# Optimization experiments

Measured on AMD Instinct MI355X. Metric: run time of the kernel, lower is better.

## Reference

```python
import jax, jax.numpy as jnp
import numpy as np

DEGREE = 3
N_KNOTS = 5

def _bspline_basis(x, t_ext, degree):
    """Vectorized Cox-de Boor. x: (..., ), t_ext: (m,) extended knots.
    Returns (..., m-1-degree) degree-`degree` basis values."""
    xe = x[..., None]
    # order-0 indicator basis: (..., m-1)
    B = ((xe >= t_ext[:-1]) & (xe < t_ext[1:])).astype(x.dtype)
    for p in range(1, degree + 1):
        left_den = t_ext[p:-1] - t_ext[:-(p + 1)]
        right_den = t_ext[p + 1:] - t_ext[1:-p]
        left = jnp.where(left_den > 0,
                         (xe - t_ext[:-(p + 1)]) / jnp.where(left_den > 0, left_den, 1.0),
                         0.0) * B[..., :-1]
        right = jnp.where(right_den > 0,
                          (t_ext[p + 1:] - xe) / jnp.where(right_den > 0, right_den, 1.0),
                          0.0) * B[..., 1:]
        B = left + right
    return B

def setup_inputs() -> dict:
    key = jax.random.key(0)
    k1, k2, k3, k4 = jax.random.split(key, 4)
    batch, input_dim, out_dim = 16384, 4096, 64
    n_coeff = N_KNOTS - DEGREE  # 2
    return {
        "x": jax.random.normal(k1, (batch, input_dim), dtype=jnp.float32),
        "c": jax.random.normal(k2, (input_dim, out_dim, n_coeff), dtype=jnp.float32),
        "ws": jax.random.normal(k3, (input_dim, out_dim), dtype=jnp.float32),
        "wb": jax.random.normal(k4, (input_dim, out_dim), dtype=jnp.float32),
    }

def reference(x, c, ws, wb):
    t = jnp.linspace(-1.0, 1.0, N_KNOTS, dtype=x.dtype)
    t_ext = jnp.concatenate([t, t[-1:]])  # pad so basis count == n_knots - degree
    # B: (batch, input_dim, n_coeff); basis depends only on x, shared knots
    B = _bspline_basis(x, t_ext, DEGREE)
    spline = jnp.einsum('bik,ijk->bj', B, c * ws[:, :, None])
    silu_mix = jax.nn.silu(x) @ wb  # sum_i wb[i,j] * x_i*sigmoid(x_i)
    return spline + silu_mix
```

## Files before the change

kernel.cpp:

```cpp
#include <hip/hip_runtime.h>
#include <hip/hip_bf16.h>
#include <stdint.h>

#define BATCH   16384
#define IN_DIM  4096
#define OUT_DIM 64
#define MTILES  (BATCH/64)

#define KI2     32
#define NCH2    (IN_DIM/KI2)
#define SPLITK  8
#define CPB2    (NCH2/SPLITK)
#define GRAN2   (OUT_DIM*13)
#define CH2W    (GRAN2*8)

#define KI      64
#define KCH     (3*KI)
#define NCHUNK  (IN_DIM/KI)
#define FCPB    16
#define CHW     (OUT_DIM*KCH)

typedef __attribute__((ext_vector_type(8))) short   short8;
typedef __attribute__((ext_vector_type(4))) float   floatx4;
typedef __attribute__((ext_vector_type(4))) uint32_t uintx4;

static __device__ __forceinline__ unsigned short f2bf(float f) {
    union { float f; uint32_t u; } v; v.f = f;
    uint32_t r = v.u + 0x7FFFu + ((v.u >> 16) & 1u);
    return (unsigned short)(r >> 16);
}

static __device__ __forceinline__ uint32_t pk2bf(float lo, float hi) {
    union { float f; uint32_t u; } a, b;
    a.f = lo; b.f = hi;
    uint32_t ra = a.u + 0x7FFFu + ((a.u >> 16) & 1u);
    uint32_t rb = b.u + 0x7FFFu + ((b.u >> 16) & 1u);
    return (ra >> 16) | (rb & 0xFFFF0000u);
}

static __device__ __forceinline__ void kan_features(float xv, float& b0, float& b1, float& sl) {
    float ax  = fabsf(xv);
    float axc = fminf(ax, 1.0f);
    float a2  = axc*axc;
    float om  = 1.0f - axc;
    float inner = __builtin_fmaf(__builtin_fmaf(4.0f, axc, -4.0f), a2, (2.0f/3.0f));
    float outer = (om*om) * (om * (4.0f/3.0f));
    b0 = (axc < 0.5f) ? inner : outer;
    float xc  = fminf(fmaxf(xv, -0.5f), 1.0f);
    float c3  = (xc < 0.0f) ? (4.0f/3.0f) : (-14.0f/3.0f);
    float mid = __builtin_fmaf(__builtin_fmaf(__builtin_fmaf(c3, xc, 2.0f), xc, 1.0f), xc, (1.0f/6.0f));
    float hi  = __builtin_fmaf(__builtin_fmaf(__builtin_fmaf(22.0f, xc, -48.0f), xc, 30.0f), xc, -4.0f) * (1.0f/3.0f);
    b1 = (xc < 0.5f) ? mid : hi;
    float e = __expf(-xv);
    sl = xv * __builtin_amdgcn_rcpf(1.0f + e);
}

__global__ __launch_bounds__(256) void kan_prep(
        const float* __restrict__ c, const float* __restrict__ ws,
        const float* __restrict__ wb, unsigned short* __restrict__ Wt) {
    int idx = blockIdx.x * 256 + threadIdx.x;
    int row = idx >> 9;
    int i   = (idx & 511) << 3;
    int j   = row / 3;
    int t   = row - j*3;
    int ci  = i >> 5;
    int ig  = (i & 31) >> 3;
    unsigned short pk[8];
    #pragma unroll
    for (int e = 0; e < 8; e++) {
        int ii = i + e;
        float v;
        if (t < 2) v = c[(size_t)ii*(OUT_DIM*2) + j*2 + t] * ws[(size_t)ii*OUT_DIM + j];
        else       v = wb[(size_t)ii*OUT_DIM + j];
        pk[e] = f2bf(v);
    }
    uintx4 d;
    d[0] = pk[0] | ((uint32_t)pk[1] << 16);
    d[1] = pk[2] | ((uint32_t)pk[3] << 16);
    d[2] = pk[4] | ((uint32_t)pk[5] << 16);
    d[3] = pk[6] | ((uint32_t)pk[7] << 16);
    int g = j*13 + t*4 + ig;
    *(uintx4*)(Wt + (size_t)ci*CH2W + (size_t)g*8) = d;
}

__global__ __launch_bounds__(256, 6) void kan_main_pre(
    const float* __restrict__ x, const unsigned short* __restrict__ Wt,
    float* __restrict__ pbuf)
{
    __shared__ unsigned short Bs[2][CH2W];

    const int tid  = threadIdx.x;
    const int wave = tid >> 6;
    const int lane = tid & 63;
    const int m    = lane & 15;
    const int q    = lane >> 4;
    const int mt   = blockIdx.x & (MTILES - 1);
    const int kh   = blockIdx.x >> 8;
    const int row0 = mt * 64;
    const int r    = row0 + wave*16 + m;
    const float* xrow = x + (size_t)r * IN_DIM;
    const int ci0 = kh * CPB2;

    floatx4 acc[4] = {};

    floatx4 xv0 = *(const floatx4*)(xrow + ci0*KI2 + q*8);
    floatx4 xv1 = *(const floatx4*)(xrow + ci0*KI2 + q*8 + 4);

    {
        const unsigned short* gW = Wt + (size_t)ci0 * CH2W;
        #pragma unroll
        for (int p = 0; p < 3; p++) {
            int g0 = p*256 + wave*64;
            __builtin_amdgcn_global_load_lds(
                (__attribute__((address_space(1))) void*)(gW + (size_t)(g0 + lane)*8),
                (__attribute__((address_space(3))) void*)(&Bs[0][0] + (size_t)g0*8),
                16, 0, 0);
        }
        if (tid < 64)
            __builtin_amdgcn_global_load_lds(
                (__attribute__((address_space(1))) void*)(gW + (size_t)(768 + lane)*8),
                (__attribute__((address_space(3))) void*)(&Bs[0][0] + (size_t)768*8),
                16, 0, 0);
    }
    __syncthreads();

    for (int cc = 0; cc < CPB2; cc++) {
        const int buf = cc & 1;
        const int ci  = ci0 + cc;

        if (cc + 1 < CPB2) {
            const unsigned short* gW = Wt + (size_t)(ci + 1) * CH2W;
            #pragma unroll
            for (int p = 0; p < 3; p++) {
                int g0 = p*256 + wave*64;
                __builtin_amdgcn_global_load_lds(
                    (__attribute__((address_space(1))) void*)(gW + (size_t)(g0 + lane)*8),
                    (__attribute__((address_space(3))) void*)(&Bs[buf^1][0] + (size_t)g0*8),
                    16, 0, 0);
            }
            if (tid < 64)
                __builtin_amdgcn_global_load_lds(
                    (__attribute__((address_space(1))) void*)(gW + (size_t)(768 + lane)*8),
                    (__attribute__((address_space(3))) void*)(&Bs[buf^1][0] + (size_t)768*8),
                    16, 0, 0);
        }

        const int inx = (cc + 1 < CPB2) ? (ci + 1)*KI2 : ci*KI2;
        floatx4 xn0 = *(const floatx4*)(xrow + inx + q*8);
        floatx4 xn1 = *(const floatx4*)(xrow + inx + q*8 + 4);

        uintx4 afu[3];
        #pragma unroll
        for (int w = 0; w < 4; w++) {
            float v0 = (w < 2) ? xv0[w*2]     : xv1[(w-2)*2];
            float v1 = (w < 2) ? xv0[w*2 + 1] : xv1[(w-2)*2 + 1];
            float b00, b10, s0, b01, b11, s1;
            kan_features(v0, b00, b10, s0);
            kan_features(v1, b01, b11, s1);
            afu[0][w] = pk2bf(b00, b01);
            afu[1][w] = pk2bf(b10, b11);
            afu[2][w] = pk2bf(s0, s1);
        }

        #pragma unroll
        for (int t = 0; t < 3; t++) {
            #pragma unroll
            for (int n = 0; n < 4; n++) {
                const int j = n*16 + m;
                short8 bf = *(const short8*)&Bs[buf][(size_t)(j*13 + t*4 + q)*8];
                acc[n] = __builtin_amdgcn_mfma_f32_16x16x32_bf16(
                    __builtin_bit_cast(short8, afu[t]), bf, acc[n], 0, 0, 0);
            }
        }

        xv0 = xn0; xv1 = xn1;
        __syncthreads();
    }

    float* pb = pbuf + (((size_t)kh*MTILES + mt)*4)*1024;
    #pragma unroll
    for (int n = 0; n < 4; n++)
        *(floatx4*)(pb + ((size_t)n*256 + tid)*4) = acc[n];
}

__global__ __launch_bounds__(256) void kan_reduce(
    const float* __restrict__ pbuf, float* __restrict__ out)
{
    const int mt   = blockIdx.x;
    const int tid  = threadIdx.x;
    const int wave = tid >> 6;
    const int lane = tid & 63;
    const int m    = lane & 15;
    const int q    = lane >> 4;
    #pragma unroll
    for (int n = 0; n < 4; n++) {
        floatx4 s = {};
        #pragma unroll
        for (int p = 0; p < SPLITK; p++) {
            floatx4 v = *(const floatx4*)(pbuf +
                (((size_t)p*MTILES + mt)*4 + n)*1024 + (size_t)tid*4);
            s += v;
        }
        #pragma unroll
        for (int reg = 0; reg < 4; reg++) {
            int orow = mt*64 + wave*16 + q*4 + reg;
            out[(size_t)orow*OUT_DIM + n*16 + m] = s[reg];
        }
    }
}

__global__ __launch_bounds__(256, 4) void kan_main_fb(
    const float* __restrict__ x, const float* __restrict__ c,
    const float* __restrict__ ws, const float* __restrict__ wb,
    float* __restrict__ out)
{
    __shared__ unsigned short Bsf[CHW];
    const int tid  = threadIdx.x;
    const int wave = tid >> 6;
    const int lane = tid & 63;
    const int m    = lane & 15;
    const int q    = lane >> 4;
    const int mt   = blockIdx.x & (MTILES - 1);
    const int kh   = blockIdx.x >> 8;
    const int row0 = mt * 64;
    const int r    = row0 + wave*16 + m;
    const float* xrow = x + (size_t)r * IN_DIM;
    floatx4 acc[4] = {};
    for (int cc = 0; cc < FCPB; cc++) {
        const int i0 = (kh * FCPB + cc) * KI;
        floatx4 xv[4];
        xv[0] = *(const floatx4*)(xrow + i0 + q*8);
        xv[1] = *(const floatx4*)(xrow + i0 + q*8 + 4);
        xv[2] = *(const floatx4*)(xrow + i0 + 32 + q*8);
        xv[3] = *(const floatx4*)(xrow + i0 + 32 + q*8 + 4);
        uintx4 afu[6];
        #pragma unroll
        for (int g = 0; g < 2; g++) {
            #pragma unroll
            for (int w = 0; w < 4; w++) {
                float v0 = xv[g*2 + (w >> 1)][(w & 1)*2 + 0];
                float v1 = xv[g*2 + (w >> 1)][(w & 1)*2 + 1];
                float b00, b10, sl0, b01, b11, sl1;
                kan_features(v0, b00, b10, sl0);
                kan_features(v1, b01, b11, sl1);
                afu[0 + g][w] = pk2bf(b00, b01);
                afu[2 + g][w] = pk2bf(b10, b11);
                afu[4 + g][w] = pk2bf(sl0, sl1);
            }
        }
        __syncthreads();
        #pragma unroll
        for (int p = 0; p < 16; p++) {
            int idx = tid + p*256;
            int j = idx & 63, i = idx >> 6;
            int gi = i0 + i;
            const float* cp = c + ((size_t)gi*OUT_DIM + j)*2;
            float c0 = cp[0], c1 = cp[1];
            float sw = ws[(size_t)gi*OUT_DIM + j];
            float b  = wb[(size_t)gi*OUT_DIM + j];
            int jx = j & 7;
            Bsf[j*KCH + ((0*8 + (i>>3)) ^ jx)*8 + (i&7)] = f2bf(c0*sw);
            Bsf[j*KCH + ((1*8 + (i>>3)) ^ jx)*8 + (i&7)] = f2bf(c1*sw);
            Bsf[j*KCH + ((2*8 + (i>>3)) ^ jx)*8 + (i&7)] = f2bf(b);
        }
        __syncthreads();
        #pragma unroll
        for (int s = 0; s < 6; s++) {
            const int kb = (s >> 1)*8 + (s & 1)*4 + q;
            #pragma unroll
            for (int n = 0; n < 4; n++) {
                const int j = n*16 + m;
                short8 bf = *(const short8*)&Bsf[j*KCH + ((kb ^ (j & 7)) << 3)];
                acc[n] = __builtin_amdgcn_mfma_f32_16x16x32_bf16(
                    __builtin_bit_cast(short8, afu[s]), bf, acc[n], 0, 0, 0);
            }
        }
    }
    #pragma unroll
    for (int n = 0; n < 4; n++)
        #pragma unroll
        for (int reg = 0; reg < 4; reg++) {
            int orow = row0 + wave*16 + q*4 + reg;
            atomicAdd(&out[(size_t)orow*OUT_DIM + n*16 + m], acc[n][reg]);
        }
}

extern "C" void kernel_launch(void* const* d_in, const int* in_sizes, int n_in,
                              void* d_out, int out_size, void* d_ws, size_t ws_size,
                              hipStream_t stream) {
    const float* x  = (const float*)d_in[0];
    const float* c  = (const float*)d_in[1];
    const float* ws = (const float*)d_in[2];
    const float* wb = (const float*)d_in[3];
    float* out = (float*)d_out;

    const size_t part_bytes = (size_t)SPLITK * BATCH * OUT_DIM * sizeof(float);
    const size_t wt_bytes   = (size_t)NCH2 * CH2W * sizeof(unsigned short);
    if (ws_size >= part_bytes + wt_bytes) {
        float* pbuf = (float*)d_ws;
        unsigned short* Wt = (unsigned short*)((char*)d_ws + part_bytes);
        kan_prep<<<384, 256, 0, stream>>>(c, ws, wb, Wt);
        kan_main_pre<<<MTILES * SPLITK, 256, 0, stream>>>(x, Wt, pbuf);
        kan_reduce<<<MTILES, 256, 0, stream>>>(pbuf, out);
    } else {
        hipMemsetAsync(d_out, 0, (size_t)out_size * sizeof(float), stream);
        kan_main_fb<<<MTILES * 4, 256, 0, stream>>>(x, c, ws, wb, out);
    }
}
```

Before: 402.8 us.

## Unroll main loop with explicit vmcnt waits and hardware bf16 pack conversion

Replaces the software round-to-nearest bf16 packing with the v_cvt_pk_bf16_f32 instruction. Unrolls the main split-K loop two chunks at a time with compile-time buffer indices. Replaces __syncthreads with inline-asm loads of the next x slice, partial vmcnt waits and a raw s_barrier, so the weight staging for the next chunk can stay in flight across the barrier. The tail staging load is also spread across all four waves instead of one. This relies on hand-counted outstanding-load numbers, which are fragile if the compiler reorders memory operations.

```diff
diff --git a/kernel.cpp b/kernel.cpp
--- a/kernel.cpp
+++ b/kernel.cpp
@@ -30,12 +30,10 @@
     return (unsigned short)(r >> 16);
 }
 
-static __device__ __forceinline__ uint32_t pk2bf(float lo, float hi) {
-    union { float f; uint32_t u; } a, b;
-    a.f = lo; b.f = hi;
-    uint32_t ra = a.u + 0x7FFFu + ((a.u >> 16) & 1u);
-    uint32_t rb = b.u + 0x7FFFu + ((b.u >> 16) & 1u);
-    return (ra >> 16) | (rb & 0xFFFF0000u);
+static __device__ __forceinline__ uint32_t pkrn(float lo, float hi) {
+    uint32_t r;
+    asm("v_cvt_pk_bf16_f32 %0, %1, %2" : "=v"(r) : "v"(lo), "v"(hi));
+    return r;
 }
 
 static __device__ __forceinline__ void kan_features(float xv, float& b0, float& b1, float& sl) {
@@ -65,22 +63,96 @@
     int t   = row - j*3;
     int ci  = i >> 5;
     int ig  = (i & 31) >> 3;
-    unsigned short pk[8];
+    float vv[8];
     #pragma unroll
     for (int e = 0; e < 8; e++) {
         int ii = i + e;
-        float v;
-        if (t < 2) v = c[(size_t)ii*(OUT_DIM*2) + j*2 + t] * ws[(size_t)ii*OUT_DIM + j];
-        else       v = wb[(size_t)ii*OUT_DIM + j];
-        pk[e] = f2bf(v);
+        if (t < 2) vv[e] = c[(size_t)ii*(OUT_DIM*2) + j*2 + t] * ws[(size_t)ii*OUT_DIM + j];
+        else       vv[e] = wb[(size_t)ii*OUT_DIM + j];
     }
     uintx4 d;
-    d[0] = pk[0] | ((uint32_t)pk[1] << 16);
-    d[1] = pk[2] | ((uint32_t)pk[3] << 16);
-    d[2] = pk[4] | ((uint32_t)pk[5] << 16);
-    d[3] = pk[6] | ((uint32_t)pk[7] << 16);
+    d[0] = pkrn(vv[0], vv[1]);
+    d[1] = pkrn(vv[2], vv[3]);
+    d[2] = pkrn(vv[4], vv[5]);
+    d[3] = pkrn(vv[6], vv[7]);
     int g = j*13 + t*4 + ig;
     *(uintx4*)(Wt + (size_t)ci*CH2W + (size_t)g*8) = d;
+}
+
+static __device__ __forceinline__ void stage_chunk(
+    const unsigned short* __restrict__ gW, unsigned short* dst,
+    int wave, int lane)
+{
+    #pragma unroll
+    for (int p = 0; p < 3; p++) {
+        int g0 = p*256 + wave*64;
+        __builtin_amdgcn_global_load_lds(
+            (__attribute__((address_space(1))) void*)(gW + (size_t)(g0 + lane)*8),
+            (__attribute__((address_space(3))) void*)(dst + (size_t)g0*8),
+            16, 0, 0);
+    }
+    if (lane < 16)
+        __builtin_amdgcn_global_load_lds(
+            (__attribute__((address_space(1))) void*)(gW + (size_t)(768 + wave*16 + lane)*8),
+            (__attribute__((address_space(3))) void*)(dst + (size_t)(768 + wave*16)*8),
+            16, 0, 0);
+}
+
+template<int BUF, bool DO_NEXT>
+static __device__ __forceinline__ void chunk_body(
+    int ci, const float* __restrict__ xrow,
+    const unsigned short* __restrict__ Wt,
+    unsigned short (&Bs)[2][CH2W],
+    int wave, int lane, int m, int q,
+    floatx4& xv0, floatx4& xv1, floatx4& xn0, floatx4& xn1,
+    floatx4 (&acc)[4])
+{
+    if constexpr (DO_NEXT) {
+        stage_chunk(Wt + (size_t)(ci + 1) * CH2W, &Bs[BUF ^ 1][0], wave, lane);
+        __builtin_amdgcn_sched_barrier(0);
+        const float* xp = xrow + (size_t)(ci + 1) * KI2 + q * 8;
+        asm volatile(
+            "global_load_dwordx4 %0, %2, off\n\t"
+            "global_load_dwordx4 %1, %2, off offset:16"
+            : "=&v"(xn0), "=&v"(xn1)
+            : "v"(xp));
+        asm volatile("s_waitcnt vmcnt(6)");
+    } else {
+        asm volatile("s_waitcnt vmcnt(0)");
+    }
+    __builtin_amdgcn_sched_barrier(0);
+
+    uintx4 afu[3];
+    #pragma unroll
+    for (int w = 0; w < 4; w++) {
+        float v0 = (w < 2) ? xv0[w*2]     : xv1[(w-2)*2];
+        float v1 = (w < 2) ? xv0[w*2 + 1] : xv1[(w-2)*2 + 1];
+        float b00, b10, s0, b01, b11, s1;
+        kan_features(v0, b00, b10, s0);
+        kan_features(v1, b01, b11, s1);
+        afu[0][w] = pkrn(b00, b01);
+        afu[1][w] = pkrn(b10, b11);
+        afu[2][w] = pkrn(s0, s1);
+    }
+
+    #pragma unroll
+    for (int t = 0; t < 3; t++) {
+        #pragma unroll
+        for (int n = 0; n < 4; n++) {
+            const int j = n*16 + m;
+            short8 bf = *(const short8*)&Bs[BUF][(size_t)(j*13 + t*4 + q)*8];
+            acc[n] = __builtin_amdgcn_mfma_f32_16x16x32_bf16(
+                __builtin_bit_cast(short8, afu[t]), bf, acc[n], 0, 0, 0);
+        }
+    }
+
+    if constexpr (DO_NEXT) {
+        __builtin_amdgcn_sched_barrier(0);
+        asm volatile("s_waitcnt vmcnt(2)");
+        __builtin_amdgcn_sched_barrier(0);
+        __builtin_amdgcn_s_barrier();
+        __builtin_amdgcn_sched_barrier(0);
+    }
 }
 
 __global__ __launch_bounds__(256, 6) void kan_main_pre(
@@ -96,8 +168,7 @@
     const int q    = lane >> 4;
     const int mt   = blockIdx.x & (MTILES - 1);
     const int kh   = blockIdx.x >> 8;
-    const int row0 = mt * 64;
-    const int r    = row0 + wave*16 + m;
+    const int r    = mt*64 + wave*16 + m;
     const float* xrow = x + (size_t)r * IN_DIM;
     const int ci0 = kh * CPB2;
 
@@ -105,77 +176,17 @@
 
     floatx4 xv0 = *(const floatx4*)(xrow + ci0*KI2 + q*8);
     floatx4 xv1 = *(const floatx4*)(xrow + ci0*KI2 + q*8 + 4);
-
-    {
-        const unsigned short* gW = Wt + (size_t)ci0 * CH2W;
-        #pragma unroll
-        for (int p = 0; p < 3; p++) {
-            int g0 = p*256 + wave*64;
-            __builtin_amdgcn_global_load_lds(
-                (__attribute__((address_space(1))) void*)(gW + (size_t)(g0 + lane)*8),
-                (__attribute__((address_space(3))) void*)(&Bs[0][0] + (size_t)g0*8),
-                16, 0, 0);
-        }
-        if (tid < 64)
-            __builtin_amdgcn_global_load_lds(
-                (__attribute__((address_space(1))) void*)(gW + (size_t)(768 + lane)*8),
-                (__attribute__((address_space(3))) void*)(&Bs[0][0] + (size_t)768*8),
-                16, 0, 0);
-    }
+    floatx4 xn0 = {}, xn1 = {};
+
+    stage_chunk(Wt + (size_t)ci0 * CH2W, &Bs[0][0], wave, lane);
     __syncthreads();
 
-    for (int cc = 0; cc < CPB2; cc++) {
-        const int buf = cc & 1;
-        const int ci  = ci0 + cc;
-
-        if (cc + 1 < CPB2) {
-            const unsigned short* gW = Wt + (size_t)(ci + 1) * CH2W;
-            #pragma unroll
-            for (int p = 0; p < 3; p++) {
-                int g0 = p*256 + wave*64;
-                __builtin_amdgcn_global_load_lds(
-                    (__attribute__((address_space(1))) void*)(gW + (size_t)(g0 + lane)*8),
-                    (__attribute__((address_space(3))) void*)(&Bs[buf^1][0] + (size_t)g0*8),
-                    16, 0, 0);
-            }
-            if (tid < 64)
-                __builtin_amdgcn_global_load_lds(
-                    (__attribute__((address_space(1))) void*)(gW + (size_t)(768 + lane)*8),
-                    (__attribute__((address_space(3))) void*)(&Bs[buf^1][0] + (size_t)768*8),
-                    16, 0, 0);
-        }
-
-        const int inx = (cc + 1 < CPB2) ? (ci + 1)*KI2 : ci*KI2;
-        floatx4 xn0 = *(const floatx4*)(xrow + inx + q*8);
-        floatx4 xn1 = *(const floatx4*)(xrow + inx + q*8 + 4);
-
-        uintx4 afu[3];
-        #pragma unroll
-        for (int w = 0; w < 4; w++) {
-            float v0 = (w < 2) ? xv0[w*2]     : xv1[(w-2)*2];
-            float v1 = (w < 2) ? xv0[w*2 + 1] : xv1[(w-2)*2 + 1];
-            float b00, b10, s0, b01, b11, s1;
-            kan_features(v0, b00, b10, s0);
-            kan_features(v1, b01, b11, s1);
-            afu[0][w] = pk2bf(b00, b01);
-            afu[1][w] = pk2bf(b10, b11);
-            afu[2][w] = pk2bf(s0, s1);
-        }
-
-        #pragma unroll
-        for (int t = 0; t < 3; t++) {
-            #pragma unroll
-            for (int n = 0; n < 4; n++) {
-                const int j = n*16 + m;
-                short8 bf = *(const short8*)&Bs[buf][(size_t)(j*13 + t*4 + q)*8];
-                acc[n] = __builtin_amdgcn_mfma_f32_16x16x32_bf16(
-                    __builtin_bit_cast(short8, afu[t]), bf, acc[n], 0, 0, 0);
-            }
-        }
-
-        xv0 = xn0; xv1 = xn1;
-        __syncthreads();
-    }
+    for (int cp = 0; cp < CPB2 - 2; cp += 2) {
+        chunk_body<0, true>(ci0+cp,   xrow, Wt, Bs, wave, lane, m, q, xv0, xv1, xn0, xn1, acc);
+        chunk_body<1, true>(ci0+cp+1, xrow, Wt, Bs, wave, lane, m, q, xn0, xn1, xv0, xv1, acc);
+    }
+    chunk_body<0, true >(ci0+CPB2-2, xrow, Wt, Bs, wave, lane, m, q, xv0, xv1, xn0, xn1, acc);
+    chunk_body<1, false>(ci0+CPB2-1, xrow, Wt, Bs, wave, lane, m, q, xn0, xn1, xv0, xv1, acc);
 
     float* pb = pbuf + (((size_t)kh*MTILES + mt)*4)*1024;
     #pragma unroll
@@ -243,9 +254,9 @@
                 float b00, b10, sl0, b01, b11, sl1;
                 kan_features(v0, b00, b10, sl0);
                 kan_features(v1, b01, b11, sl1);
-                afu[0 + g][w] = pk2bf(b00, b01);
-                afu[2 + g][w] = pk2bf(b10, b11);
-                afu[4 + g][w] = pk2bf(sl0, sl1);
+                afu[0 + g][w] = pkrn(b00, b01);
+                afu[2 + g][w] = pkrn(b10, b11);
+                afu[4 + g][w] = pkrn(sl0, sl1);
             }
         }
         __syncthreads();
@@ -303,7 +314,7 @@
         kan_main_pre<<<MTILES * SPLITK, 256, 0, stream>>>(x, Wt, pbuf);
         kan_reduce<<<MTILES, 256, 0, stream>>>(pbuf, out);
     } else {
-        hipMemsetAsync(d_out, 0, (size_t)out_size * sizeof(float), stream);
+        (void)hipMemsetAsync(d_out, 0, (size_t)out_size * sizeof(float), stream);
         kan_main_fb<<<MTILES * 4, 256, 0, stream>>>(x, c, ws, wb, out);
     }
 }
```

Result: slower. 420.7 us (+4.4%).
